# Performance work log

Measured on AMD Instinct MI355X. Metric: run time of the kernel, lower is better.

Reference implementation:

```python
import jax, jax.numpy as jnp
import numpy as np

D_MODEL = 1024
N_HEAD = 16
HEAD_D = D_MODEL // N_HEAD
D_FF = 4096
LN_EPS = 1e-5
ATTN_EPS = 1e-6


def _layer_norm(x, g, b, eps=LN_EPS):
    mu = jnp.mean(x, axis=-1, keepdims=True)
    var = jnp.var(x, axis=-1, keepdims=True)
    return (x - mu) * jax.lax.rsqrt(var + eps) * g + b


def setup_inputs() -> dict:
    key = jax.random.key(0)
    ks = jax.random.split(key, 16)
    s = 0.02
    return {
        "src": jax.random.normal(ks[0], (4, 4096, D_MODEL), dtype=jnp.float32),
        "qkv_w": jax.random.normal(ks[1], (D_MODEL, 3 * D_MODEL), dtype=jnp.float32) * s,
        "qkv_b": jax.random.normal(ks[2], (3 * D_MODEL,), dtype=jnp.float32) * s,
        "out_w": jax.random.normal(ks[3], (D_MODEL, D_MODEL), dtype=jnp.float32) * s,
        "out_b": jax.random.normal(ks[4], (D_MODEL,), dtype=jnp.float32) * s,
        "w1": jax.random.normal(ks[5], (D_MODEL, D_FF), dtype=jnp.float32) * s,
        "b1": jax.random.normal(ks[6], (D_FF,), dtype=jnp.float32) * s,
        "w2": jax.random.normal(ks[7], (D_FF, D_MODEL), dtype=jnp.float32) * s,
        "b2": jax.random.normal(ks[8], (D_MODEL,), dtype=jnp.float32) * s,
        "g1": jnp.ones((D_MODEL,), dtype=jnp.float32),
        "be1": jnp.zeros((D_MODEL,), dtype=jnp.float32),
        "g2": jnp.ones((D_MODEL,), dtype=jnp.float32),
        "be2": jnp.zeros((D_MODEL,), dtype=jnp.float32),
    }


def _linear_attention(x, qkv_w, qkv_b, out_w, out_b):
    B, N, C = x.shape
    qkv = (x @ qkv_w + qkv_b).reshape(B, N, 3, N_HEAD, HEAD_D)
    qkv = jnp.transpose(qkv, (2, 0, 3, 1, 4))  # [3,B,H,N,D]
    q, k, v = qkv[0], qkv[1], qkv[2]
    # phi = elu(x) + 1 (positive feature map)
    qf = jax.nn.elu(q) + 1.0
    kf = jax.nn.elu(k) + 1.0
    # kv aggregation: [B,H,D,D]
    kv = jnp.einsum('bhnd,bhne->bhde', kf.astype(jnp.float32), v.astype(jnp.float32)).astype(v.dtype)
    y_num = jnp.einsum('bhnd,bhde->bhne', qf, kv)  # [B,H,N,D]
    z = jnp.sum(kf.astype(jnp.float32), axis=2)  # [B,H,D]
    y_den = jnp.einsum('bhnd,bhd->bhn', qf, z.astype(qf.dtype))
    y_den = jnp.maximum(y_den, ATTN_EPS)[..., None]
    y = (y_num / y_den).transpose(0, 2, 1, 3).reshape(B, N, C)
    return y @ out_w + out_b


def reference(src, qkv_w, qkv_b, out_w, out_b, w1, b1, w2, b2, g1, be1, g2, be2):
    # pre-norm (norm_first=True), dropout disabled (eval)
    attn_out = _linear_attention(_layer_norm(src, g1, be1), qkv_w, qkv_b, out_w, out_b)
    x = src + attn_out
    h = jax.nn.gelu(_layer_norm(x, g2, be2) @ w1 + b1, approximate=False)
    return x + h @ w2 + b2
```

## Files before the change

kernel.cpp:

```cpp
#include <hip/hip_runtime.h>
#include <hip/hip_bf16.h>
#include <math.h>

typedef __attribute__((ext_vector_type(8))) short short8;
typedef __attribute__((ext_vector_type(4))) float floatx4;

__device__ __forceinline__ float bf2f(unsigned int u) {
    union { unsigned int i; float f; } c; c.i = u << 16; return c.f;
}
__device__ __forceinline__ unsigned short f2bf(float f) {
    unsigned int x = __builtin_bit_cast(unsigned int, f);
    unsigned int r = (x + 0x7fffu + ((x >> 16) & 1u)) >> 16;
    return (unsigned short)r;
}
__device__ __forceinline__ float elu1(float x) { return x > 0.f ? x + 1.f : __expf(x); }
__device__ __forceinline__ float gelu_exact(float x) {
    return 0.5f * x * (1.f + erff(x * 0.70710678118654752f));
}

__device__ __forceinline__ void async_cp16(const void* g, void* l) {
    __builtin_amdgcn_global_load_lds(
        (const __attribute__((address_space(1))) unsigned int*)g,
        (__attribute__((address_space(3))) unsigned int*)l, 16, 0, 0);
}

__global__ void zero_f32(float* __restrict__ p, int n) {
    int i = blockIdx.x * 256 + threadIdx.x;
    if (i < n) p[i] = 0.f;
}

__global__ void wcvt(const float* __restrict__ in, unsigned short* __restrict__ outp,
                     int K, int N) {
    __shared__ float tile[32][33];
    const int n0 = blockIdx.x * 32, k0 = blockIdx.y * 32;
    const int tx = threadIdx.x, ty = threadIdx.y;
#pragma unroll
    for (int i = 0; i < 4; i++)
        tile[ty + 8 * i][tx] = in[(size_t)(k0 + ty + 8 * i) * N + n0 + tx];
    __syncthreads();
#pragma unroll
    for (int i = 0; i < 4; i++)
        outp[(size_t)(n0 + ty + 8 * i) * K + k0 + tx] = f2bf(tile[tx][ty + 8 * i]);
}

__global__ __launch_bounds__(256)
void ln_kernel(const float* __restrict__ x, const float* __restrict__ g,
               const float* __restrict__ be, unsigned short* __restrict__ out) {
    const int row = blockIdx.x;
    const int t = threadIdx.x;
    const float4 v = *(const float4*)(x + (size_t)row * 1024 + t * 4);
    float s = v.x + v.y + v.z + v.w;
    float s2 = v.x * v.x + v.y * v.y + v.z * v.z + v.w * v.w;
#pragma unroll
    for (int off = 32; off > 0; off >>= 1) {
        s += __shfl_down(s, off);
        s2 += __shfl_down(s2, off);
    }
    __shared__ float red[8];
    __shared__ float stat[2];
    const int w = t >> 6, l = t & 63;
    if (l == 0) { red[w] = s; red[4 + w] = s2; }
    __syncthreads();
    if (t == 0) {
        float S = red[0] + red[1] + red[2] + red[3];
        float S2 = red[4] + red[5] + red[6] + red[7];
        float mu = S * (1.f / 1024.f);
        float var = S2 * (1.f / 1024.f) - mu * mu;
        stat[0] = mu;
        stat[1] = rsqrtf(var + 1e-5f);
    }
    __syncthreads();
    const float mu = stat[0], rs = stat[1];
    const float4 gv = *(const float4*)(g + t * 4);
    const float4 bv = *(const float4*)(be + t * 4);
    unsigned int o0 = f2bf((v.x - mu) * rs * gv.x + bv.x);
    unsigned int o1 = f2bf((v.y - mu) * rs * gv.y + bv.y);
    unsigned int o2 = f2bf((v.z - mu) * rs * gv.z + bv.z);
    unsigned int o3 = f2bf((v.w - mu) * rs * gv.w + bv.w);
    uint2 pk;
    pk.x = o0 | (o1 << 16);
    pk.y = o2 | (o3 << 16);
    *(uint2*)(out + (size_t)row * 1024 + t * 4) = pk;
}

template <int EPI>
__global__ __launch_bounds__(256, 2)
void gemm_bt(const unsigned short* __restrict__ A, const unsigned short* __restrict__ B,
             const float* __restrict__ bias, const float* __restrict__ resid,
             unsigned short* __restrict__ Cbf, float* __restrict__ Cf32,
             int N, int K) {
    __shared__ unsigned short At[128 * 32];
    __shared__ unsigned short Bt[128 * 32];
    const int t = threadIdx.x;
    const int l = t & 63;
    const int w = t >> 6;
    const int m0 = blockIdx.y * 128;
    const int n0 = blockIdx.x * 128;
    const int wm = (w >> 1) * 64;
    const int wn = (w & 1) * 64;

    floatx4 acc[4][4];
    const floatx4 zz = {0.f, 0.f, 0.f, 0.f};
#pragma unroll
    for (int i = 0; i < 4; i++)
#pragma unroll
        for (int j = 0; j < 4; j++) acc[i][j] = zz;

    const int sr = t >> 2;
    const int sc = (t & 3) << 3;
    const unsigned short* ag = A + (size_t)(m0 + sr) * K + sc;
    const unsigned short* ag2 = ag + (size_t)64 * K;
    const unsigned short* bg = B + (size_t)(n0 + sr) * K + sc;
    const unsigned short* bg2 = bg + (size_t)64 * K;
    unsigned short* la = At + t * 8;
    unsigned short* la2 = At + 2048 + t * 8;
    unsigned short* lb = Bt + t * 8;
    unsigned short* lb2 = Bt + 2048 + t * 8;

    const int fr = l & 15;
    const int fo = (l >> 4) << 3;

    for (int k0 = 0; k0 < K; k0 += 32) {
        async_cp16(ag + k0, la);
        async_cp16(ag2 + k0, la2);
        async_cp16(bg + k0, lb);
        async_cp16(bg2 + k0, lb2);
        __syncthreads();
        short8 af[4], bf[4];
#pragma unroll
        for (int i = 0; i < 4; i++)
            af[i] = *(const short8*)(At + (wm + i * 16 + fr) * 32 + fo);
#pragma unroll
        for (int i = 0; i < 4; i++)
            bf[i] = *(const short8*)(Bt + (wn + i * 16 + fr) * 32 + fo);
#pragma unroll
        for (int i = 0; i < 4; i++)
#pragma unroll
            for (int j = 0; j < 4; j++)
                acc[i][j] = __builtin_amdgcn_mfma_f32_16x16x32_bf16(af[i], bf[j], acc[i][j], 0, 0, 0);
        __syncthreads();
    }

    const int er = (l >> 4) << 2;
    const int ec = l & 15;
#pragma unroll
    for (int j = 0; j < 4; j++) {
        const int col = n0 + wn + j * 16 + ec;
        const float bb = bias[col];
#pragma unroll
        for (int i = 0; i < 4; i++) {
            const int rowb = m0 + wm + i * 16 + er;
#pragma unroll
            for (int r = 0; r < 4; r++) {
                const int row = rowb + r;
                float v = acc[i][j][r] + bb;
                const size_t idx = (size_t)row * N + col;
                if (EPI == 0) {
                    if (col < 2048) v = elu1(v);
                    Cbf[idx] = f2bf(v);
                } else if (EPI == 1) {
                    Cf32[idx] = v + resid[idx];
                } else {
                    Cbf[idx] = f2bf(gelu_exact(v));
                }
            }
        }
    }
}

__global__ __launch_bounds__(256)
void kv_kernel(const unsigned short* __restrict__ qkv, float* __restrict__ kvz) {
    const int bh = blockIdx.x;
    const int chunk = blockIdx.y;
    const int b = bh >> 4, h = bh & 15;
    const int t = threadIdx.x;
    __shared__ float kf[64][68];
    __shared__ float vv[64][68];
    const int te = t >> 4, td = t & 15;
    float acc[4][4];
#pragma unroll
    for (int i = 0; i < 4; i++)
#pragma unroll
        for (int j = 0; j < 4; j++) acc[i][j] = 0.f;
    float zacc = 0.f;
    const size_t base = (size_t)b * 4096 * 3072 + (size_t)chunk * 512 * 3072;
    const int koff = 1024 + h * 64;
    const int voff = 2048 + h * 64;
    const int rl = t >> 3, seg = t & 7;

    for (int s = 0; s < 8; s++) {
#pragma unroll
        for (int p = 0; p < 2; p++) {
            const int nl = p * 32 + rl;
            const unsigned short* rp = qkv + base + (size_t)(s * 64 + nl) * 3072;
            const uint4 kd = *(const uint4*)(rp + koff + seg * 8);
            const uint4 vd = *(const uint4*)(rp + voff + seg * 8);
            float* kdst = &kf[nl][seg * 8];
            float* vdst = &vv[nl][seg * 8];
            kdst[0] = bf2f(kd.x & 0xffff); kdst[1] = bf2f(kd.x >> 16);
            kdst[2] = bf2f(kd.y & 0xffff); kdst[3] = bf2f(kd.y >> 16);
            kdst[4] = bf2f(kd.z & 0xffff); kdst[5] = bf2f(kd.z >> 16);
            kdst[6] = bf2f(kd.w & 0xffff); kdst[7] = bf2f(kd.w >> 16);
            vdst[0] = bf2f(vd.x & 0xffff); vdst[1] = bf2f(vd.x >> 16);
            vdst[2] = bf2f(vd.y & 0xffff); vdst[3] = bf2f(vd.y >> 16);
            vdst[4] = bf2f(vd.z & 0xffff); vdst[5] = bf2f(vd.z >> 16);
            vdst[6] = bf2f(vd.w & 0xffff); vdst[7] = bf2f(vd.w >> 16);
        }
        __syncthreads();
        for (int n = 0; n < 64; n++) {
            const float4 kk = *(const float4*)&kf[n][te * 4];
            const float4 vn = *(const float4*)&vv[n][td * 4];
            const float ka[4] = {kk.x, kk.y, kk.z, kk.w};
            const float va[4] = {vn.x, vn.y, vn.z, vn.w};
#pragma unroll
            for (int i = 0; i < 4; i++)
#pragma unroll
                for (int j = 0; j < 4; j++) acc[i][j] = fmaf(ka[i], va[j], acc[i][j]);
        }
        if (t < 64) {
            for (int n = 0; n < 64; n++) zacc += kf[n][t];
        }
        __syncthreads();
    }
    float* kvp = kvz + bh * 4160;
#pragma unroll
    for (int i = 0; i < 4; i++)
#pragma unroll
        for (int j = 0; j < 4; j++)
            atomicAdd(&kvp[(te * 4 + i) * 64 + td * 4 + j], acc[i][j]);
    if (t < 64) atomicAdd(&kvp[4096 + t], zacc);
}

__global__ __launch_bounds__(256)
void y_kernel(const unsigned short* __restrict__ qkv, const float* __restrict__ kvz,
              unsigned short* __restrict__ y) {
    const int bh = blockIdx.x, chunk = blockIdx.y;
    const int b = bh >> 4, h = bh & 15;
    const int t = threadIdx.x;
    __shared__ float kv[64][68];
    __shared__ float zs[64];
    __shared__ float qf[16][68];
    const float* kvp = kvz + bh * 4160;
#pragma unroll
    for (int p = 0; p < 4; p++) {
        const int f = (t + p * 256) * 4;
        const float4 v4 = *(const float4*)(kvp + f);
        *(float4*)&kv[f >> 6][f & 63] = v4;
    }
    if (t < 16) *(float4*)&zs[t * 4] = *(const float4*)(kvp + 4096 + t * 4);
    __syncthreads();
    const int nl = t >> 4, td = t & 15;
    const size_t base = (size_t)b * 4096 * 3072 + (size_t)chunk * 128 * 3072;
    const int qoff = h * 64;
    for (int s = 0; s < 8; s++) {
        if (t < 128) {
            const int r = t >> 3, seg = t & 7;
            const uint4 qd = *(const uint4*)(qkv + base + (size_t)(s * 16 + r) * 3072 + qoff + seg * 8);
            float* qdst = &qf[r][seg * 8];
            qdst[0] = bf2f(qd.x & 0xffff); qdst[1] = bf2f(qd.x >> 16);
            qdst[2] = bf2f(qd.y & 0xffff); qdst[3] = bf2f(qd.y >> 16);
            qdst[4] = bf2f(qd.z & 0xffff); qdst[5] = bf2f(qd.z >> 16);
            qdst[6] = bf2f(qd.w & 0xffff); qdst[7] = bf2f(qd.w >> 16);
        }
        __syncthreads();
        float a0 = 0.f, a1 = 0.f, a2 = 0.f, a3 = 0.f, den = 0.f;
        for (int e = 0; e < 64; e++) {
            const float q = qf[nl][e];
            const float4 kvv = *(const float4*)&kv[e][td * 4];
            a0 = fmaf(q, kvv.x, a0);
            a1 = fmaf(q, kvv.y, a1);
            a2 = fmaf(q, kvv.z, a2);
            a3 = fmaf(q, kvv.w, a3);
            den = fmaf(q, zs[e], den);
        }
        const float inv = 1.f / fmaxf(den, 1e-6f);
        const int tok = b * 4096 + chunk * 128 + s * 16 + nl;
        unsigned int o0 = f2bf(a0 * inv), o1 = f2bf(a1 * inv);
        unsigned int o2 = f2bf(a2 * inv), o3 = f2bf(a3 * inv);
        uint2 pk;
        pk.x = o0 | (o1 << 16);
        pk.y = o2 | (o3 << 16);
        *(uint2*)(y + (size_t)tok * 1024 + h * 64 + td * 4) = pk;
        __syncthreads();
    }
}

extern "C" void kernel_launch(void* const* d_in, const int* in_sizes, int n_in,
                              void* d_out, int out_size, void* d_ws, size_t ws_size,
                              hipStream_t stream) {
    const float* src   = (const float*)d_in[0];
    const float* qkv_w = (const float*)d_in[1];
    const float* qkv_b = (const float*)d_in[2];
    const float* out_w = (const float*)d_in[3];
    const float* out_b = (const float*)d_in[4];
    const float* w1    = (const float*)d_in[5];
    const float* b1    = (const float*)d_in[6];
    const float* w2    = (const float*)d_in[7];
    const float* b2    = (const float*)d_in[8];
    const float* g1    = (const float*)d_in[9];
    const float* be1   = (const float*)d_in[10];
    const float* g2    = (const float*)d_in[11];
    const float* be2   = (const float*)d_in[12];
    float* outp = (float*)d_out;

    char* ws = (char*)d_ws;
    unsigned short* qkvwT = (unsigned short*)(ws + 0);
    unsigned short* outwT = (unsigned short*)(ws + 6291456);
    unsigned short* w1T   = (unsigned short*)(ws + 8388608);
    unsigned short* w2T   = (unsigned short*)(ws + 16777216);
    unsigned short* bufA  = (unsigned short*)(ws + 25165824);
    unsigned short* bufB  = (unsigned short*)(ws + 159383552);
    float*          xbuf  = (float*)(ws + 192937984);
    float*          kvz   = (float*)(ws + 260046848);

    wcvt<<<dim3(3072 / 32, 1024 / 32), dim3(32, 8), 0, stream>>>(qkv_w, qkvwT, 1024, 3072);
    wcvt<<<dim3(1024 / 32, 1024 / 32), dim3(32, 8), 0, stream>>>(out_w, outwT, 1024, 1024);
    wcvt<<<dim3(4096 / 32, 1024 / 32), dim3(32, 8), 0, stream>>>(w1, w1T, 1024, 4096);
    wcvt<<<dim3(1024 / 32, 4096 / 32), dim3(32, 8), 0, stream>>>(w2, w2T, 4096, 1024);
    zero_f32<<<(266240 + 255) / 256, 256, 0, stream>>>(kvz, 266240);

    ln_kernel<<<16384, 256, 0, stream>>>(src, g1, be1, bufB);
    gemm_bt<0><<<dim3(24, 128), 256, 0, stream>>>(bufB, qkvwT, qkv_b, nullptr, bufA, nullptr, 3072, 1024);
    kv_kernel<<<dim3(64, 8), 256, 0, stream>>>(bufA, kvz);
    y_kernel<<<dim3(64, 32), 256, 0, stream>>>(bufA, kvz, bufB);
    gemm_bt<1><<<dim3(8, 128), 256, 0, stream>>>(bufB, outwT, out_b, src, nullptr, xbuf, 1024, 1024);
    ln_kernel<<<16384, 256, 0, stream>>>(xbuf, g2, be2, bufB);
    gemm_bt<2><<<dim3(32, 128), 256, 0, stream>>>(bufB, w1T, b1, nullptr, bufA, nullptr, 4096, 1024);
    gemm_bt<1><<<dim3(8, 128), 256, 0, stream>>>(bufA, w2T, b2, xbuf, nullptr, outp, 1024, 4096);
}
```

Measured before the change: 921.9 us.

## Fuse weight prep kernels, remap GEMM blocks per XCD, raise occupancy bound

Merges the four weight transpose/convert launches and the zero fill into one prep kernel, removing launch gaps. Remaps GEMM block indices so consecutive tiles land on the same XCD, aiming at better L2 reuse on MI355X's chiplet layout. Raises the GEMM launch bound to 4 blocks per CU, which may cap registers and risk spills.

Result: faster. 882.6 us (-4.3%).

```diff
diff --git a/kernel.cpp b/kernel.cpp
--- a/kernel.cpp
+++ b/kernel.cpp
@@ -24,23 +24,36 @@
         (__attribute__((address_space(3))) unsigned int*)l, 16, 0, 0);
 }
 
-__global__ void zero_f32(float* __restrict__ p, int n) {
-    int i = blockIdx.x * 256 + threadIdx.x;
-    if (i < n) p[i] = 0.f;
-}
-
-__global__ void wcvt(const float* __restrict__ in, unsigned short* __restrict__ outp,
-                     int K, int N) {
+__global__ void prep_kernel(const float* __restrict__ qkv_w, const float* __restrict__ out_w,
+                            const float* __restrict__ w1, const float* __restrict__ w2,
+                            unsigned short* __restrict__ qkvwT, unsigned short* __restrict__ outwT,
+                            unsigned short* __restrict__ w1T, unsigned short* __restrict__ w2T,
+                            float* __restrict__ kvz) {
+    const int bid = blockIdx.x;
+    const int tx = threadIdx.x, ty = threadIdx.y;
+    if (bid >= 12288) {
+        const int lid = ty * 32 + tx;
+        const int i = (bid - 12288) * 1024 + lid * 4;
+        *(float4*)(kvz + i) = make_float4(0.f, 0.f, 0.f, 0.f);
+        return;
+    }
+    const float* in;
+    unsigned short* op;
+    int K, N, tb;
+    if (bid < 3072)      { in = qkv_w; op = qkvwT; K = 1024; N = 3072; tb = bid; }
+    else if (bid < 4096) { in = out_w; op = outwT; K = 1024; N = 1024; tb = bid - 3072; }
+    else if (bid < 8192) { in = w1;    op = w1T;   K = 1024; N = 4096; tb = bid - 4096; }
+    else                 { in = w2;    op = w2T;   K = 4096; N = 1024; tb = bid - 8192; }
+    const int nx = N >> 5;
+    const int n0 = (tb % nx) * 32, k0 = (tb / nx) * 32;
     __shared__ float tile[32][33];
-    const int n0 = blockIdx.x * 32, k0 = blockIdx.y * 32;
-    const int tx = threadIdx.x, ty = threadIdx.y;
 #pragma unroll
     for (int i = 0; i < 4; i++)
         tile[ty + 8 * i][tx] = in[(size_t)(k0 + ty + 8 * i) * N + n0 + tx];
     __syncthreads();
 #pragma unroll
     for (int i = 0; i < 4; i++)
-        outp[(size_t)(n0 + ty + 8 * i) * K + k0 + tx] = f2bf(tile[tx][ty + 8 * i]);
+        op[(size_t)(n0 + ty + 8 * i) * K + k0 + tx] = f2bf(tile[tx][ty + 8 * i]);
 }
 
 __global__ __launch_bounds__(256)
@@ -84,7 +97,7 @@
 }
 
 template <int EPI>
-__global__ __launch_bounds__(256, 2)
+__global__ __launch_bounds__(256, 4)
 void gemm_bt(const unsigned short* __restrict__ A, const unsigned short* __restrict__ B,
              const float* __restrict__ bias, const float* __restrict__ resid,
              unsigned short* __restrict__ Cbf, float* __restrict__ Cf32,
@@ -94,8 +107,18 @@
     const int t = threadIdx.x;
     const int l = t & 63;
     const int w = t >> 6;
-    const int m0 = blockIdx.y * 128;
-    const int n0 = blockIdx.x * 128;
+
+    const int T = gridDim.x * gridDim.y;
+    const int f = blockIdx.y * gridDim.x + blockIdx.x;
+    int bx = blockIdx.x, by = blockIdx.y;
+    if ((T & 7) == 0) {
+        const int per = T >> 3;
+        const int g = (f & 7) * per + (f >> 3);
+        bx = g % gridDim.x;
+        by = g / gridDim.x;
+    }
+    const int m0 = by * 128;
+    const int n0 = bx * 128;
     const int wm = (w >> 1) * 64;
     const int wn = (w & 1) * 64;
 
@@ -313,11 +336,8 @@
     float*          xbuf  = (float*)(ws + 192937984);
     float*          kvz   = (float*)(ws + 260046848);
 
-    wcvt<<<dim3(3072 / 32, 1024 / 32), dim3(32, 8), 0, stream>>>(qkv_w, qkvwT, 1024, 3072);
-    wcvt<<<dim3(1024 / 32, 1024 / 32), dim3(32, 8), 0, stream>>>(out_w, outwT, 1024, 1024);
-    wcvt<<<dim3(4096 / 32, 1024 / 32), dim3(32, 8), 0, stream>>>(w1, w1T, 1024, 4096);
-    wcvt<<<dim3(1024 / 32, 4096 / 32), dim3(32, 8), 0, stream>>>(w2, w2T, 4096, 1024);
-    zero_f32<<<(266240 + 255) / 256, 256, 0, stream>>>(kvz, 266240);
+    prep_kernel<<<12548, dim3(32, 8), 0, stream>>>(qkv_w, out_w, w1, w2,
+                                                   qkvwT, outwT, w1T, w2T, kvz);
 
     ln_kernel<<<16384, 256, 0, stream>>>(src, g1, be1, bufB);
     gemm_bt<0><<<dim3(24, 128), 256, 0, stream>>>(bufB, qkvwT, qkv_b, nullptr, bufA, nullptr, 3072, 1024);
```
